# Kernel optimization log

Hardware: AMD Instinct MI355X
Metric: run time of the kernel (lower is better)

Reference implementation:

```python
import jax, jax.numpy as jnp
import numpy as np

NUM_CHUNKS = 8
TOP_K = 2
IN_F = 4096
HID_F = 4096
OUT_F = 4096
B = 4096


def setup_inputs() -> dict:
    key = jax.random.key(0)
    k = jax.random.split(key, 5)
    cin = IN_F // NUM_CHUNKS    # 512
    cout = HID_F // NUM_CHUNKS  # 512
    s_in = 1.0 / np.sqrt(cin)
    s_fin = 1.0 / np.sqrt(cout * TOP_K)
    return {
        "x": jax.random.normal(k[0], (B, IN_F), dtype=jnp.float32),
        # stacked chunk-expert Linear params: y = x @ W + b
        "W_chunks": jax.random.uniform(k[1], (NUM_CHUNKS, cin, cout), jnp.float32, -s_in, s_in),
        "b_chunks": jax.random.uniform(k[2], (NUM_CHUNKS, cout), jnp.float32, -s_in, s_in),
        "W_final": jax.random.uniform(k[3], (cout * TOP_K, OUT_F), jnp.float32, -s_fin, s_fin),
        "b_final": jax.random.uniform(k[4], (OUT_F,), jnp.float32, -s_fin, s_fin),
    }


def reference(x, W_chunks, b_chunks, W_final, b_final):
    Bsz = x.shape[0]
    # split into chunks along feature dim: (B, num_chunks, chunk_in)
    xr = x.reshape(Bsz, NUM_CHUNKS, -1)
    # per-chunk activity = mean(|chunk|) over the whole batch (matches torch .abs().mean())
    activities = jnp.mean(jnp.abs(xr), axis=(0, 2))  # (num_chunks,)
    _, topk_idx = jax.lax.top_k(activities, TOP_K)    # descending, like torch.topk
    # gather selected chunks and their expert weights, run small GEMMs
    x_sel = xr[:, topk_idx, :]                        # (B, k, chunk_in)
    h = jnp.einsum('bkc,kcd->bkd', x_sel, W_chunks[topk_idx]) + b_chunks[topk_idx]
    h = h.reshape(Bsz, -1)                            # concat along feature dim
    out = h @ W_final + b_final                       # (B, out_features)
    return out
```

## Files before the change

kernel.cpp:

```cpp
#include <hip/hip_runtime.h>


typedef __bf16 bf16x8_t __attribute__((ext_vector_type(8)));
typedef float  f32x4_t  __attribute__((ext_vector_type(4)));
typedef unsigned short u16x4 __attribute__((ext_vector_type(4)));

__device__ inline unsigned short f2bf(float f) {
    __bf16 b = (__bf16)f;
    return __builtin_bit_cast(unsigned short, b);
}

__device__ inline void stage_glds(const unsigned short* gtile, int stride, int row0,
                                  unsigned short* lds, int lane) {
    const int r8 = lane >> 3;
    const int gg = (lane & 7) ^ r8;
    const unsigned short* gp = gtile + (size_t)(row0 + r8) * stride + gg * 8;
    unsigned short* lp = lds + row0 * 64;
    __builtin_amdgcn_global_load_lds((const __attribute__((address_space(1))) void*)gp,
                                     (__attribute__((address_space(3))) void*)lp,
                                     16, 0, 0);
}

__device__ inline bf16x8_t ldsfrag(const unsigned short* Ls, int row, int kb) {
    return *(const bf16x8_t*)(Ls + row * 64 + (((kb >> 3) ^ (row & 7)) * 8));
}

__global__ void fused_prep_kernel(const float* __restrict__ x, const float* __restrict__ Wc,
                                  const float* __restrict__ Wf, float* __restrict__ part,
                                  unsigned short* __restrict__ wct, unsigned short* __restrict__ wft) {
    const int b = blockIdx.x;
    const int tid = threadIdx.x;

    if (b < 512) {
        const int chunk = b & 7;
        const int rg = b >> 3;
        const int colf4 = tid & 127;
        const int rsub = tid >> 7;
        const float4* base = (const float4*)x + (size_t)chunk * 128 + colf4;
        float s = 0.f;
        #pragma unroll 4
        for (int i = 0; i < 32; ++i) {
            int row = rg * 64 + i * 2 + rsub;
            float4 v = base[(size_t)row * 1024];
            s += fabsf(v.x) + fabsf(v.y) + fabsf(v.z) + fabsf(v.w);
        }
        #pragma unroll
        for (int off = 32; off > 0; off >>= 1) s += __shfl_down(s, off, 64);
        __shared__ float wsum[4];
        if ((tid & 63) == 0) wsum[tid >> 6] = s;
        __syncthreads();
        if (tid == 0) part[chunk * 64 + rg] = wsum[0] + wsum[1] + wsum[2] + wsum[3];
        return;
    }

    __shared__ float tile[32][33];
    const int tx = tid & 31, ty = tid >> 5;
    const float* src; unsigned short* dst; int R, C, cb, rb;
    int jj = b - 512;
    if (jj < 4096) {
        src = Wf; dst = wft; R = 1024; C = 4096;
        cb = (jj & 127) * 32; rb = (jj >> 7) * 32;
    } else {
        jj -= 4096;
        int c = jj >> 8, t = jj & 255;
        src = Wc + (size_t)c * 262144;
        dst = wct + (size_t)c * 262144;
        R = 512; C = 512;
        cb = (t & 15) * 32; rb = (t >> 4) * 32;
    }
    #pragma unroll
    for (int i = 0; i < 4; ++i)
        tile[ty + i * 8][tx] = src[(size_t)(rb + ty + i * 8) * C + cb + tx];
    __syncthreads();
    {
        const int tx8  = tid & 7;
        const int ty32 = tid >> 3;
        u16x4 hv;
        #pragma unroll
        for (int j = 0; j < 4; ++j) hv[j] = f2bf(tile[tx8 * 4 + j][ty32]);
        *(u16x4*)(dst + (size_t)(cb + ty32) * R + rb + tx8 * 4) = hv;
    }
}

__global__ __launch_bounds__(256, 4)
void gemm1_kernel(const float* __restrict__ x, const unsigned short* __restrict__ wct,
                  const float* __restrict__ bc, const float* __restrict__ part,
                  unsigned short* __restrict__ h) {
    __shared__ __align__(16) unsigned char lds_raw[24576];
    unsigned short* As = (unsigned short*)lds_raw;
    unsigned short* Bs = (unsigned short*)(lds_raw + 8192);

    const int tid = threadIdx.x;
    const int wave = tid >> 6;
    const int lane = tid & 63;

    {
        float* sred = (float*)lds_raw;
        sred[tid] = part[tid];
        sred[tid + 256] = part[tid + 256];
        __syncthreads();
        float* act8 = (float*)(lds_raw + 2048);
        if (tid < 8) {
            float a = 0.f;
            #pragma unroll
            for (int k = 0; k < 64; ++k) a += sred[tid * 64 + k];
            act8[tid] = a;
        }
        __syncthreads();
    }
    int sel0, sel1;
    {
        const float* act8 = (const float*)(lds_raw + 2048);
        float v0 = -1e30f, v1 = -1e30f; int b0 = 0, b1 = 0;
        #pragma unroll
        for (int i = 0; i < 8; ++i) {
            float v = act8[i];
            if (v > v0) { v1 = v0; b1 = b0; v0 = v; b0 = i; }
            else if (v > v1) { v1 = v; b1 = i; }
        }
        sel0 = b0; sel1 = b1;
    }
    __syncthreads();

    const int z = blockIdx.z;
    const int idxz = z ? sel1 : sel0;
    const int m0 = blockIdx.x * 64;
    const int n0 = blockIdx.y * 128;
    const int wm = (wave >> 1) * 32;
    const int wn = (wave & 1) * 64;
    const int rl = lane & 15;
    const int quad = lane >> 4;

    const float* xtile = x + (size_t)m0 * 4096 + idxz * 512;
    const unsigned short* Btile = wct + (size_t)idxz * 262144 + (size_t)n0 * 512;

    f32x4_t acc[4][2] = {};
    const int ar = tid >> 2;
    const int aq = tid & 3;

    for (int k0 = 0; k0 < 512; k0 += 64) {
        #pragma unroll
        for (int s = wave; s < 16; s += 4)
            stage_glds(Btile + k0, 512, s * 8, Bs, lane);
        const float* gr = xtile + (size_t)ar * 4096 + k0;
        #pragma unroll
        for (int j = 0; j < 2; ++j) {
            int gg = aq * 2 + j;
            float4 a = *(const float4*)(gr + gg * 8);
            float4 c = *(const float4*)(gr + gg * 8 + 4);
            bf16x8_t v;
            v[0] = (__bf16)a.x; v[1] = (__bf16)a.y; v[2] = (__bf16)a.z; v[3] = (__bf16)a.w;
            v[4] = (__bf16)c.x; v[5] = (__bf16)c.y; v[6] = (__bf16)c.z; v[7] = (__bf16)c.w;
            *(bf16x8_t*)(As + ar * 64 + ((gg ^ (ar & 7)) * 8)) = v;
        }
        __syncthreads();
        #pragma unroll
        for (int kq = 0; kq < 2; ++kq) {
            const int kb = kq * 32 + quad * 8;
            bf16x8_t af[2], bfr[4];
            #pragma unroll
            for (int i = 0; i < 2; ++i) af[i]  = ldsfrag(As, wm + i * 16 + rl, kb);
            #pragma unroll
            for (int i = 0; i < 4; ++i) bfr[i] = ldsfrag(Bs, wn + i * 16 + rl, kb);
            #pragma unroll
            for (int ni = 0; ni < 4; ++ni)
                #pragma unroll
                for (int mi = 0; mi < 2; ++mi)
                    acc[ni][mi] = __builtin_amdgcn_mfma_f32_16x16x32_bf16(bfr[ni], af[mi], acc[ni][mi], 0, 0, 0);
        }
        __syncthreads();
    }

    const float* bias = bc + (size_t)idxz * 512;
    #pragma unroll
    for (int ni = 0; ni < 4; ++ni) {
        const int colb = n0 + wn + ni * 16 + quad * 4;
        f32x4_t bv4 = *(const f32x4_t*)(bias + colb);
        #pragma unroll
        for (int mi = 0; mi < 2; ++mi) {
            int row = m0 + wm + mi * 16 + rl;
            f32x4_t o = acc[ni][mi] + bv4;
            u16x4 hv;
            #pragma unroll
            for (int j = 0; j < 4; ++j) hv[j] = f2bf(o[j]);
            *(u16x4*)(h + (size_t)row * 1024 + z * 512 + colb) = hv;
        }
    }
}

__global__ __launch_bounds__(256, 4)
void gemm2_kernel(const unsigned short* __restrict__ h, const unsigned short* __restrict__ wft,
                  const float* __restrict__ bfin, float* __restrict__ out) {
    __shared__ __align__(16) unsigned short As[128 * 64];
    __shared__ __align__(16) unsigned short Bs[128 * 64];
    const int m0 = blockIdx.x * 128;
    const int n0 = blockIdx.y * 128;
    const int tid = threadIdx.x;
    const int wave = tid >> 6;
    const int lane = tid & 63;
    const int wm = (wave >> 1) * 64;
    const int wn = (wave & 1) * 64;
    const int rl = lane & 15;
    const int quad = lane >> 4;

    const unsigned short* Atile = h + (size_t)m0 * 1024;
    const unsigned short* Btile = wft + (size_t)n0 * 1024;

    f32x4_t acc[4][4] = {};

    for (int k0 = 0; k0 < 1024; k0 += 64) {
        #pragma unroll
        for (int s = wave; s < 32; s += 4) {
            if (s < 16) stage_glds(Atile + k0, 1024, s * 8, As, lane);
            else        stage_glds(Btile + k0, 1024, (s - 16) * 8, Bs, lane);
        }
        __syncthreads();
        #pragma unroll
        for (int kq = 0; kq < 2; ++kq) {
            const int kb = kq * 32 + quad * 8;
            bf16x8_t af[4], bfr[4];
            #pragma unroll
            for (int i = 0; i < 4; ++i) {
                af[i]  = ldsfrag(As, wm + i * 16 + rl, kb);
                bfr[i] = ldsfrag(Bs, wn + i * 16 + rl, kb);
            }
            #pragma unroll
            for (int ni = 0; ni < 4; ++ni)
                #pragma unroll
                for (int mi = 0; mi < 4; ++mi)
                    acc[ni][mi] = __builtin_amdgcn_mfma_f32_16x16x32_bf16(bfr[ni], af[mi], acc[ni][mi], 0, 0, 0);
        }
        __syncthreads();
    }

    #pragma unroll
    for (int ni = 0; ni < 4; ++ni) {
        const int colb = n0 + wn + ni * 16 + quad * 4;
        f32x4_t bv4 = *(const f32x4_t*)(bfin + colb);
        #pragma unroll
        for (int mi = 0; mi < 4; ++mi) {
            int row = m0 + wm + mi * 16 + rl;
            f32x4_t o = acc[ni][mi] + bv4;
            *(f32x4_t*)(out + (size_t)row * 4096 + colb) = o;
        }
    }
}

extern "C" void kernel_launch(void* const* d_in, const int* in_sizes, int n_in,
                              void* d_out, int out_size, void* d_ws, size_t ws_size,
                              hipStream_t stream) {
    const float* x    = (const float*)d_in[0];
    const float* Wc   = (const float*)d_in[1];
    const float* bc   = (const float*)d_in[2];
    const float* Wf   = (const float*)d_in[3];
    const float* bfin = (const float*)d_in[4];
    float* out = (float*)d_out;

    float* part = (float*)d_ws;
    unsigned short* h   = (unsigned short*)((char*)d_ws + 4096);
    unsigned short* wct = h   + (size_t)4096 * 1024;
    unsigned short* wft = wct + (size_t)8 * 512 * 512;

    fused_prep_kernel<<<6656, 256, 0, stream>>>(x, Wc, Wf, part, wct, wft);
    gemm1_kernel<<<dim3(64, 4, 2), 256, 0, stream>>>(x, wct, bc, part, h);
    gemm2_kernel<<<dim3(32, 32, 1), 256, 0, stream>>>(h, wft, bfin, out);
}
```

Baseline: 184.5 us.

## Double-buffer both GEMMs, pre-cast x to bf16, swizzle gemm2 block order

```diff
diff --git a/kernel.cpp b/kernel.cpp
--- a/kernel.cpp
+++ b/kernel.cpp
@@ -27,7 +27,8 @@
 
 __global__ void fused_prep_kernel(const float* __restrict__ x, const float* __restrict__ Wc,
                                   const float* __restrict__ Wf, float* __restrict__ part,
-                                  unsigned short* __restrict__ wct, unsigned short* __restrict__ wft) {
+                                  unsigned short* __restrict__ wct, unsigned short* __restrict__ wft,
+                                  unsigned short* __restrict__ xbf) {
     const int b = blockIdx.x;
     const int tid = threadIdx.x;
 
@@ -37,12 +38,16 @@
         const int colf4 = tid & 127;
         const int rsub = tid >> 7;
         const float4* base = (const float4*)x + (size_t)chunk * 128 + colf4;
+        unsigned short* xdst = xbf + (size_t)chunk * 512 + colf4 * 4;
         float s = 0.f;
         #pragma unroll 4
         for (int i = 0; i < 32; ++i) {
             int row = rg * 64 + i * 2 + rsub;
             float4 v = base[(size_t)row * 1024];
             s += fabsf(v.x) + fabsf(v.y) + fabsf(v.z) + fabsf(v.w);
+            u16x4 hv;
+            hv[0] = f2bf(v.x); hv[1] = f2bf(v.y); hv[2] = f2bf(v.z); hv[3] = f2bf(v.w);
+            *(u16x4*)(xdst + (size_t)row * 4096) = hv;
         }
         #pragma unroll
         for (int off = 32; off > 0; off >>= 1) s += __shfl_down(s, off, 64);
@@ -82,13 +87,11 @@
     }
 }
 
-__global__ __launch_bounds__(256, 4)
-void gemm1_kernel(const float* __restrict__ x, const unsigned short* __restrict__ wct,
+__global__ __launch_bounds__(256, 3)
+void gemm1_kernel(const unsigned short* __restrict__ xbf, const unsigned short* __restrict__ wct,
                   const float* __restrict__ bc, const float* __restrict__ part,
                   unsigned short* __restrict__ h) {
-    __shared__ __align__(16) unsigned char lds_raw[24576];
-    unsigned short* As = (unsigned short*)lds_raw;
-    unsigned short* Bs = (unsigned short*)(lds_raw + 8192);
+    __shared__ __align__(16) unsigned char lds_raw[49152];
 
     const int tid = threadIdx.x;
     const int wave = tid >> 6;
@@ -131,37 +134,40 @@
     const int rl = lane & 15;
     const int quad = lane >> 4;
 
-    const float* xtile = x + (size_t)m0 * 4096 + idxz * 512;
+    const unsigned short* Atile = xbf + (size_t)m0 * 4096 + idxz * 512;
     const unsigned short* Btile = wct + (size_t)idxz * 262144 + (size_t)n0 * 512;
 
     f32x4_t acc[4][2] = {};
-    const int ar = tid >> 2;
-    const int aq = tid & 3;
-
-    for (int k0 = 0; k0 < 512; k0 += 64) {
-        #pragma unroll
-        for (int s = wave; s < 16; s += 4)
-            stage_glds(Btile + k0, 512, s * 8, Bs, lane);
-        const float* gr = xtile + (size_t)ar * 4096 + k0;
-        #pragma unroll
-        for (int j = 0; j < 2; ++j) {
-            int gg = aq * 2 + j;
-            float4 a = *(const float4*)(gr + gg * 8);
-            float4 c = *(const float4*)(gr + gg * 8 + 4);
-            bf16x8_t v;
-            v[0] = (__bf16)a.x; v[1] = (__bf16)a.y; v[2] = (__bf16)a.z; v[3] = (__bf16)a.w;
-            v[4] = (__bf16)c.x; v[5] = (__bf16)c.y; v[6] = (__bf16)c.z; v[7] = (__bf16)c.w;
-            *(bf16x8_t*)(As + ar * 64 + ((gg ^ (ar & 7)) * 8)) = v;
-        }
-        __syncthreads();
+
+    #pragma unroll
+    for (int s = wave; s < 8; s += 4)
+        stage_glds(Atile, 4096, s * 8, (unsigned short*)lds_raw, lane);
+    #pragma unroll
+    for (int s = wave; s < 16; s += 4)
+        stage_glds(Btile, 512, s * 8, (unsigned short*)(lds_raw + 16384), lane);
+    __syncthreads();
+
+    for (int t = 0; t < 8; ++t) {
+        const int cb = t & 1;
+        unsigned short* Ascur = (unsigned short*)(lds_raw + cb * 8192);
+        unsigned short* Bscur = (unsigned short*)(lds_raw + 16384 + cb * 16384);
+        if (t < 7) {
+            unsigned short* Asnxt = (unsigned short*)(lds_raw + (cb ^ 1) * 8192);
+            unsigned short* Bsnxt = (unsigned short*)(lds_raw + 16384 + (cb ^ 1) * 16384);
+            const int k1 = (t + 1) * 64;
+            #pragma unroll
+            for (int s = wave; s < 8; s += 4)  stage_glds(Atile + k1, 4096, s * 8, Asnxt, lane);
+            #pragma unroll
+            for (int s = wave; s < 16; s += 4) stage_glds(Btile + k1, 512,  s * 8, Bsnxt, lane);
+        }
         #pragma unroll
         for (int kq = 0; kq < 2; ++kq) {
             const int kb = kq * 32 + quad * 8;
             bf16x8_t af[2], bfr[4];
             #pragma unroll
-            for (int i = 0; i < 2; ++i) af[i]  = ldsfrag(As, wm + i * 16 + rl, kb);
-            #pragma unroll
-            for (int i = 0; i < 4; ++i) bfr[i] = ldsfrag(Bs, wn + i * 16 + rl, kb);
+            for (int i = 0; i < 2; ++i) af[i]  = ldsfrag(Ascur, wm + i * 16 + rl, kb);
+            #pragma unroll
+            for (int i = 0; i < 4; ++i) bfr[i] = ldsfrag(Bscur, wn + i * 16 + rl, kb);
             #pragma unroll
             for (int ni = 0; ni < 4; ++ni)
                 #pragma unroll
@@ -188,13 +194,17 @@
     }
 }
 
-__global__ __launch_bounds__(256, 4)
+__global__ __launch_bounds__(256, 2)
 void gemm2_kernel(const unsigned short* __restrict__ h, const unsigned short* __restrict__ wft,
                   const float* __restrict__ bfin, float* __restrict__ out) {
-    __shared__ __align__(16) unsigned short As[128 * 64];
-    __shared__ __align__(16) unsigned short Bs[128 * 64];
-    const int m0 = blockIdx.x * 128;
-    const int n0 = blockIdx.y * 128;
+    __shared__ __align__(16) unsigned short As[2][128 * 64];
+    __shared__ __align__(16) unsigned short Bs[2][128 * 64];
+
+    const int f = blockIdx.x;
+    const int g = (f & 7) * 128 + (f >> 3);
+    const int m0 = (g & 31) * 128;
+    const int n0 = (g >> 5) * 128;
+
     const int tid = threadIdx.x;
     const int wave = tid >> 6;
     const int lane = tid & 63;
@@ -208,21 +218,31 @@
 
     f32x4_t acc[4][4] = {};
 
-    for (int k0 = 0; k0 < 1024; k0 += 64) {
-        #pragma unroll
-        for (int s = wave; s < 32; s += 4) {
-            if (s < 16) stage_glds(Atile + k0, 1024, s * 8, As, lane);
-            else        stage_glds(Btile + k0, 1024, (s - 16) * 8, Bs, lane);
-        }
-        __syncthreads();
+    #pragma unroll
+    for (int s = wave; s < 32; s += 4) {
+        if (s < 16) stage_glds(Atile, 1024, s * 8, As[0], lane);
+        else        stage_glds(Btile, 1024, (s - 16) * 8, Bs[0], lane);
+    }
+    __syncthreads();
+
+    for (int t = 0; t < 16; ++t) {
+        const int cb = t & 1;
+        if (t < 15) {
+            const int k1 = (t + 1) * 64;
+            #pragma unroll
+            for (int s = wave; s < 32; s += 4) {
+                if (s < 16) stage_glds(Atile + k1, 1024, s * 8, As[cb ^ 1], lane);
+                else        stage_glds(Btile + k1, 1024, (s - 16) * 8, Bs[cb ^ 1], lane);
+            }
+        }
         #pragma unroll
         for (int kq = 0; kq < 2; ++kq) {
             const int kb = kq * 32 + quad * 8;
             bf16x8_t af[4], bfr[4];
             #pragma unroll
             for (int i = 0; i < 4; ++i) {
-                af[i]  = ldsfrag(As, wm + i * 16 + rl, kb);
-                bfr[i] = ldsfrag(Bs, wn + i * 16 + rl, kb);
+                af[i]  = ldsfrag(As[cb], wm + i * 16 + rl, kb);
+                bfr[i] = ldsfrag(Bs[cb], wn + i * 16 + rl, kb);
             }
             #pragma unroll
             for (int ni = 0; ni < 4; ++ni)
@@ -260,8 +280,9 @@
     unsigned short* h   = (unsigned short*)((char*)d_ws + 4096);
     unsigned short* wct = h   + (size_t)4096 * 1024;
     unsigned short* wft = wct + (size_t)8 * 512 * 512;
-
-    fused_prep_kernel<<<6656, 256, 0, stream>>>(x, Wc, Wf, part, wct, wft);
-    gemm1_kernel<<<dim3(64, 4, 2), 256, 0, stream>>>(x, wct, bc, part, h);
-    gemm2_kernel<<<dim3(32, 32, 1), 256, 0, stream>>>(h, wft, bfin, out);
-}
+    unsigned short* xbf = wft + (size_t)4096 * 1024;
+
+    fused_prep_kernel<<<6656, 256, 0, stream>>>(x, Wc, Wf, part, wct, wft, xbf);
+    gemm1_kernel<<<dim3(64, 4, 2), 256, 0, stream>>>(xbf, wct, bc, part, h);
+    gemm2_kernel<<<1024, 256, 0, stream>>>(h, wft, bfin, out);
+}
```

Result: slower. 206.7 us (+12.0%).

## Convert x to bf16 during activity pass and stage gemm1 A via global_load_lds

Applied to the files above, without the earlier changes.

```diff
diff --git a/kernel.cpp b/kernel.cpp
--- a/kernel.cpp
+++ b/kernel.cpp
@@ -27,7 +27,8 @@
 
 __global__ void fused_prep_kernel(const float* __restrict__ x, const float* __restrict__ Wc,
                                   const float* __restrict__ Wf, float* __restrict__ part,
-                                  unsigned short* __restrict__ wct, unsigned short* __restrict__ wft) {
+                                  unsigned short* __restrict__ wct, unsigned short* __restrict__ wft,
+                                  unsigned short* __restrict__ xbf) {
     const int b = blockIdx.x;
     const int tid = threadIdx.x;
 
@@ -37,12 +38,16 @@
         const int colf4 = tid & 127;
         const int rsub = tid >> 7;
         const float4* base = (const float4*)x + (size_t)chunk * 128 + colf4;
+        unsigned short* xdst = xbf + (size_t)chunk * 512 + colf4 * 4;
         float s = 0.f;
         #pragma unroll 4
         for (int i = 0; i < 32; ++i) {
             int row = rg * 64 + i * 2 + rsub;
             float4 v = base[(size_t)row * 1024];
             s += fabsf(v.x) + fabsf(v.y) + fabsf(v.z) + fabsf(v.w);
+            u16x4 hv;
+            hv[0] = f2bf(v.x); hv[1] = f2bf(v.y); hv[2] = f2bf(v.z); hv[3] = f2bf(v.w);
+            *(u16x4*)(xdst + (size_t)row * 4096) = hv;
         }
         #pragma unroll
         for (int off = 32; off > 0; off >>= 1) s += __shfl_down(s, off, 64);
@@ -83,7 +88,7 @@
 }
 
 __global__ __launch_bounds__(256, 4)
-void gemm1_kernel(const float* __restrict__ x, const unsigned short* __restrict__ wct,
+void gemm1_kernel(const unsigned short* __restrict__ xbf, const unsigned short* __restrict__ wct,
                   const float* __restrict__ bc, const float* __restrict__ part,
                   unsigned short* __restrict__ h) {
     __shared__ __align__(16) unsigned char lds_raw[24576];
@@ -131,28 +136,18 @@
     const int rl = lane & 15;
     const int quad = lane >> 4;
 
-    const float* xtile = x + (size_t)m0 * 4096 + idxz * 512;
+    const unsigned short* Atile = xbf + (size_t)m0 * 4096 + idxz * 512;
     const unsigned short* Btile = wct + (size_t)idxz * 262144 + (size_t)n0 * 512;
 
     f32x4_t acc[4][2] = {};
-    const int ar = tid >> 2;
-    const int aq = tid & 3;
 
     for (int k0 = 0; k0 < 512; k0 += 64) {
+        #pragma unroll
+        for (int s = wave; s < 8; s += 4)
+            stage_glds(Atile + k0, 4096, s * 8, As, lane);
         #pragma unroll
         for (int s = wave; s < 16; s += 4)
             stage_glds(Btile + k0, 512, s * 8, Bs, lane);
-        const float* gr = xtile + (size_t)ar * 4096 + k0;
-        #pragma unroll
-        for (int j = 0; j < 2; ++j) {
-            int gg = aq * 2 + j;
-            float4 a = *(const float4*)(gr + gg * 8);
-            float4 c = *(const float4*)(gr + gg * 8 + 4);
-            bf16x8_t v;
-            v[0] = (__bf16)a.x; v[1] = (__bf16)a.y; v[2] = (__bf16)a.z; v[3] = (__bf16)a.w;
-            v[4] = (__bf16)c.x; v[5] = (__bf16)c.y; v[6] = (__bf16)c.z; v[7] = (__bf16)c.w;
-            *(bf16x8_t*)(As + ar * 64 + ((gg ^ (ar & 7)) * 8)) = v;
-        }
         __syncthreads();
         #pragma unroll
         for (int kq = 0; kq < 2; ++kq) {
@@ -225,23 +220,27 @@
                 bfr[i] = ldsfrag(Bs, wn + i * 16 + rl, kb);
             }
             #pragma unroll
+            for (int mi = 0; mi < 4; ++mi)
+                #pragma unroll
+                for (int ni = 0; ni < 4; ++ni)
+                    acc[mi][ni] = __builtin_amdgcn_mfma_f32_16x16x32_bf16(af[mi], bfr[ni], acc[mi][ni], 0, 0, 0);
+        }
+        __syncthreads();
+    }
+
+    const int row_l = quad * 4;
+    float bv[4];
+    #pragma unroll
+    for (int ni = 0; ni < 4; ++ni) bv[ni] = bfin[n0 + wn + ni * 16 + rl];
+    #pragma unroll
+    for (int j = 0; j < 4; ++j) {
+        #pragma unroll
+        for (int mi = 0; mi < 4; ++mi) {
+            int row = m0 + wm + mi * 16 + row_l + j;
+            float* orow = out + (size_t)row * 4096 + n0 + wn + rl;
+            #pragma unroll
             for (int ni = 0; ni < 4; ++ni)
-                #pragma unroll
-                for (int mi = 0; mi < 4; ++mi)
-                    acc[ni][mi] = __builtin_amdgcn_mfma_f32_16x16x32_bf16(bfr[ni], af[mi], acc[ni][mi], 0, 0, 0);
-        }
-        __syncthreads();
-    }
-
-    #pragma unroll
-    for (int ni = 0; ni < 4; ++ni) {
-        const int colb = n0 + wn + ni * 16 + quad * 4;
-        f32x4_t bv4 = *(const f32x4_t*)(bfin + colb);
-        #pragma unroll
-        for (int mi = 0; mi < 4; ++mi) {
-            int row = m0 + wm + mi * 16 + rl;
-            f32x4_t o = acc[ni][mi] + bv4;
-            *(f32x4_t*)(out + (size_t)row * 4096 + colb) = o;
+                orow[ni * 16] = acc[mi][ni][j] + bv[ni];
         }
     }
 }
@@ -260,8 +259,9 @@
     unsigned short* h   = (unsigned short*)((char*)d_ws + 4096);
     unsigned short* wct = h   + (size_t)4096 * 1024;
     unsigned short* wft = wct + (size_t)8 * 512 * 512;
-
-    fused_prep_kernel<<<6656, 256, 0, stream>>>(x, Wc, Wf, part, wct, wft);
-    gemm1_kernel<<<dim3(64, 4, 2), 256, 0, stream>>>(x, wct, bc, part, h);
+    unsigned short* xbf = wft + (size_t)4096 * 1024;
+
+    fused_prep_kernel<<<6656, 256, 0, stream>>>(x, Wc, Wf, part, wct, wft, xbf);
+    gemm1_kernel<<<dim3(64, 4, 2), 256, 0, stream>>>(xbf, wct, bc, part, h);
     gemm2_kernel<<<dim3(32, 32, 1), 256, 0, stream>>>(h, wft, bfin, out);
 }
```

Measured after the change: 191.4 us. 3.7% more time.
